# Optimization experiments

Hardware: AMD Instinct MI355X
Metric: run time of the kernel (lower is better)

The kernel has to match this reference:

```python
import jax, jax.numpy as jnp
import numpy as np

N_EMBD = 1024
N_HEAD = 16
HEAD_SIZE = 64


def setup_inputs() -> dict:
    key = jax.random.key(0)
    ks = jax.random.split(key, 6)
    B, T, C, H, D = 2, 2048, N_EMBD, N_HEAD, HEAD_SIZE
    s = 1.0 / np.sqrt(C)
    x = jax.random.normal(ks[0], (B, T, C), dtype=jnp.float32)
    Wq = jax.random.normal(ks[1], (H, C, D), dtype=jnp.float32) * s
    Wk = jax.random.normal(ks[2], (H, C, D), dtype=jnp.float32) * s
    Wv = jax.random.normal(ks[3], (H, C, D), dtype=jnp.float32) * s
    Wo = jax.random.normal(ks[4], (H * D, C), dtype=jnp.float32) * (1.0 / np.sqrt(H * D))
    bo = jax.random.normal(ks[5], (C,), dtype=jnp.float32) * 0.01
    return {"x": x, "Wq": Wq, "Wk": Wk, "Wv": Wv, "Wo": Wo, "bo": bo}


def reference(x, Wq, Wk, Wv, Wo, bo):
    B, T, C = x.shape
    H, _, D = Wq.shape
    # Per-head projections, batched across heads: [B,H,T,D]
    q = jnp.einsum('btc,hcd->bhtd', x, Wq)
    k = jnp.einsum('btc,hcd->bhtd', x, Wk)
    v = jnp.einsum('btc,hcd->bhtd', x, Wv)
    # NOTE: original scales by sqrt(C) = sqrt(n_embd), not sqrt(head_size)
    scale = 1.0 / jnp.sqrt(jnp.float32(C))
    att = jnp.einsum('bhtd,bhsd->bhts', q, k) * scale  # [B,H,T,T]
    causal = jnp.tril(jnp.ones((T, T), dtype=bool))
    att = jnp.where(causal, att, -jnp.inf)
    att = jax.nn.softmax(att, axis=-1)
    # dropout omitted (eval mode / deterministic reference)
    out = jnp.einsum('bhts,bhsd->bhtd', att, v)  # [B,H,T,D]
    out = out.transpose(0, 2, 1, 3).reshape(B, T, H * D)
    return out @ Wo + bo
```

## Files before the change

kernel.cpp:

```cpp
#include <hip/hip_runtime.h>
#include <hip/hip_bf16.h>


typedef __hip_bfloat16 bf16;
typedef __bf16 v8bf __attribute__((ext_vector_type(8)));
typedef float  v4f  __attribute__((ext_vector_type(4)));
typedef unsigned long long u64;
typedef unsigned int u32;

#define MFMA16(a, b, c) __builtin_amdgcn_mfma_f32_16x16x32_bf16((a), (b), (c), 0, 0, 0)

__device__ __forceinline__ bf16 f2b(float x) { return __float2bfloat16(x); }
__device__ __forceinline__ __bf16 f2braw(float x) {
  bf16 t = __float2bfloat16(x);
  return *reinterpret_cast<__bf16*>(&t);
}
__device__ __forceinline__ unsigned short f2bu(float x) {
  bf16 t = __float2bfloat16(x);
  return *reinterpret_cast<unsigned short*>(&t);
}

__device__ __forceinline__ void load16_lds(const bf16* gptr, const bf16* lptr) {
  __builtin_amdgcn_global_load_lds(
      (const __attribute__((address_space(1))) u32*)gptr,
      (__attribute__((address_space(3))) u32*)lptr, 16, 0, 0);
}

__global__ __launch_bounds__(256) void prep_kernel(
    const float* __restrict__ x,
    const float* __restrict__ Wq, const float* __restrict__ Wk,
    const float* __restrict__ Wv, const float* __restrict__ Wo,
    bf16* __restrict__ xb, bf16* __restrict__ wt, bf16* __restrict__ wot)
{
  __shared__ float Lt[32][33];
  const int bid = blockIdx.x, tid = threadIdx.x;

  if (bid < 2048) {
    size_t i = ((size_t)bid * 256 + tid) * 8;
    float4 f0 = *(const float4*)(x + i);
    float4 f1 = *(const float4*)(x + i + 4);
    v8bf v;
    v[0] = f2braw(f0.x); v[1] = f2braw(f0.y); v[2] = f2braw(f0.z); v[3] = f2braw(f0.w);
    v[4] = f2braw(f1.x); v[5] = f2braw(f1.y); v[6] = f2braw(f1.z); v[7] = f2braw(f1.w);
    *(v8bf*)(xb + i) = v;
    return;
  }
  const int tx = tid & 31, ty = tid >> 5;
  if (bid < 5120) {
    const int idx = bid - 2048;
    const int z = idx >> 6, rem = idx & 63;
    const int p = z >> 4, h = z & 15;
    const float* ib = ((p == 0) ? Wq : (p == 1) ? Wk : Wv) + (size_t)h * 65536;
    bf16* ob = wt + (size_t)z * 65536;
    const int j0 = (rem & 1) * 32, i0 = (rem >> 1) * 32;
    #pragma unroll
    for (int r = 0; r < 4; ++r)
      Lt[ty + 8 * r][tx] = ib[(size_t)(i0 + ty + 8 * r) * 64 + j0 + tx];
    __syncthreads();
    #pragma unroll
    for (int r = 0; r < 4; ++r)
      ob[(size_t)(j0 + ty + 8 * r) * 1024 + i0 + tx] = f2b(Lt[tx][ty + 8 * r]);
  } else {
    const int idx = bid - 5120;
    const int j0 = (idx & 31) * 32, i0 = (idx >> 5) * 32;
    #pragma unroll
    for (int r = 0; r < 4; ++r)
      Lt[ty + 8 * r][tx] = Wo[(size_t)(i0 + ty + 8 * r) * 1024 + j0 + tx];
    __syncthreads();
    #pragma unroll
    for (int r = 0; r < 4; ++r)
      wot[(size_t)(j0 + ty + 8 * r) * 1024 + i0 + tx] = f2b(Lt[tx][ty + 8 * r]);
  }
}

__global__ __launch_bounds__(256) void qkv_gemm_kernel(
    const bf16* __restrict__ xb, const bf16* __restrict__ wt,
    bf16* __restrict__ qkv)
{
  __shared__ __align__(16) bf16 Ash[2][128][32];
  __shared__ __align__(16) bf16 Bsh[2][128][32];

  const int mt = blockIdx.x, nt = blockIdx.y;
  const int tid = threadIdx.x, w = tid >> 6, lane = tid & 63;
  const int ln = lane & 15, quad = lane >> 4;
  const int wm = w >> 1, wn = w & 1;
  const int m0 = mt * 128, n0 = nt * 128;

  const v4f vzero = {0.f, 0.f, 0.f, 0.f};
  v4f acc[4][4];
  #pragma unroll
  for (int mf = 0; mf < 4; ++mf)
    #pragma unroll
    for (int nf = 0; nf < 4; ++nf) acc[mf][nf] = vzero;

  const int srow = lane >> 2, sseg = (lane & 3) * 8;
  const bf16* ga = xb + (size_t)(m0 + 32 * w + srow) * 1024 + sseg;
  const bf16* gb = wt + (size_t)(n0 + 32 * w + srow) * 1024 + sseg;

  {
    load16_lds(ga,             &Ash[0][32 * w][0]);
    load16_lds(ga + 16 * 1024, &Ash[0][32 * w + 16][0]);
    load16_lds(gb,             &Bsh[0][32 * w][0]);
    load16_lds(gb + 16 * 1024, &Bsh[0][32 * w + 16][0]);
  }

  for (int kt = 0; kt < 32; ++kt) {
    const int buf = kt & 1;
    __syncthreads();

    v8bf af[4], bfv[4];
    #pragma unroll
    for (int mf = 0; mf < 4; ++mf)
      af[mf] = *(const v8bf*)&Ash[buf][wm * 64 + mf * 16 + ln][quad * 8];
    #pragma unroll
    for (int nf = 0; nf < 4; ++nf)
      bfv[nf] = *(const v8bf*)&Bsh[buf][wn * 64 + nf * 16 + ln][quad * 8];

    if (kt < 31) {
      const int k0 = (kt + 1) * 32, nb = buf ^ 1;
      load16_lds(ga + k0,             &Ash[nb][32 * w][0]);
      load16_lds(ga + 16 * 1024 + k0, &Ash[nb][32 * w + 16][0]);
      load16_lds(gb + k0,             &Bsh[nb][32 * w][0]);
      load16_lds(gb + 16 * 1024 + k0, &Bsh[nb][32 * w + 16][0]);
    }

    #pragma unroll
    for (int mf = 0; mf < 4; ++mf)
      #pragma unroll
      for (int nf = 0; nf < 4; ++nf)
        acc[mf][nf] = MFMA16(af[mf], bfv[nf], acc[mf][nf]);
  }

  const int jcol0 = n0 + wn * 64;
  const int p = jcol0 >> 10;
  const int h = (jcol0 >> 6) & 15;
  const float scale = (p == 0) ? 0.03125f : 1.0f;

  if (p < 2) {
    bf16* base = qkv + (size_t)p * 4194304 + (size_t)h * 262144;
    #pragma unroll
    for (int mf = 0; mf < 4; ++mf)
      #pragma unroll
      for (int nf = 0; nf < 4; ++nf) {
        int d = nf * 16 + ln;
        #pragma unroll
        for (int r = 0; r < 4; ++r) {
          int m = m0 + wm * 64 + mf * 16 + quad * 4 + r;
          base[(size_t)m * 64 + d] = f2b(acc[mf][nf][r] * scale);
        }
      }
  } else {
    bf16* vb = qkv + (size_t)2 * 4194304 + (size_t)h * 262144;
    #pragma unroll
    for (int mf = 0; mf < 4; ++mf) {
      int mrow = m0 + wm * 64 + mf * 16 + quad * 4;
      int bi = mrow >> 11, t0 = mrow & 2047;
      #pragma unroll
      for (int nf = 0; nf < 4; ++nf) {
        int d = nf * 16 + ln;
        u64 pk = (u64)f2bu(acc[mf][nf][0]) |
                 ((u64)f2bu(acc[mf][nf][1]) << 16) |
                 ((u64)f2bu(acc[mf][nf][2]) << 32) |
                 ((u64)f2bu(acc[mf][nf][3]) << 48);
        *(u64*)(vb + (size_t)bi * 131072 + (size_t)d * 2048 + t0) = pk;
      }
    }
  }
}

__global__ __launch_bounds__(256, 2) void attn_kernel(
    const bf16* __restrict__ qkv, bf16* __restrict__ att)
{
  __shared__ __align__(16) bf16 Ksh[2][64][64];
  __shared__ __align__(16) bf16 Vsh[2][64][64];

  const int fid = blockIdx.x;
  const int pairid = fid >> 5;
  const int grp = fid & 31;
  const int b = grp >> 4, h = grp & 15;

  const int tid = threadIdx.x, w = tid >> 6, lane = tid & 63;
  const int ln = lane & 15, quad = lane >> 4;

  const bf16* qbase  = qkv + (size_t)h * 262144 + (size_t)b * 131072;
  const bf16* kbase  = qbase + 4194304;
  const bf16* vtbase = qbase + 8388608;

  const int l8 = lane & 7, r8 = lane >> 3;
  const int slot = l8 ^ r8;
  const int p0 = w * 16 + r8, p1 = p0 + 8;
  const int kp0 = (p0 & 32) | ((p0 & 12) << 1) | ((p0 & 16) >> 2) | (p0 & 3);
  const int kp1 = (p1 & 32) | ((p1 & 12) << 1) | ((p1 & 16) >> 2) | (p1 & 3);
  const bf16* gk0 = kbase + kp0 * 64 + slot * 8;
  const bf16* gk1 = kbase + kp1 * 64 + slot * 8;
  const bf16* gv0 = vtbase + (w * 16 + r8) * 2048 + slot * 8;
  const bf16* gv1 = gv0 + 8 * 2048;

  const int sw = ln & 7;
  const int c0 = ((quad    ) ^ sw) * 8;
  const int c1 = ((quad + 4) ^ sw) * 8;
  const int rowoff = ln * 64;

  v8bf vone;
  {
    unsigned short u = 0x3F80;
    __bf16 e = *reinterpret_cast<__bf16*>(&u);
    #pragma unroll
    for (int j = 0; j < 8; ++j) vone[j] = e;
  }
  const v4f vzero = {0.f, 0.f, 0.f, 0.f};
  const float NEG = -30000.0f;

  #define STAGE(KB, BUF) {                                       \
    load16_lds(gk0 + (KB) * 4096, &Ksh[BUF][w * 16][0]);         \
    load16_lds(gk1 + (KB) * 4096, &Ksh[BUF][w * 16 + 8][0]);     \
    load16_lds(gv0 + (KB) * 64,   &Vsh[BUF][w * 16][0]);         \
    load16_lds(gv1 + (KB) * 64,   &Vsh[BUF][w * 16 + 8][0]); }

  #pragma unroll 1
  for (int half = 0; half < 2; ++half) {
    const int mt = half ? (31 - pairid) : pairid;
    const int row0 = mt * 64;
    const int wrow = row0 + w * 16;
    const int qg = wrow + ln;

    v8bf aq[2];
    #pragma unroll
    for (int ks = 0; ks < 2; ++ks)
      aq[ks] = *(const v8bf*)(qbase + (size_t)(wrow + ln) * 64 + ks * 32 + quad * 8);

    v4f o[4], lacc;
    lacc = vzero;
    #pragma unroll
    for (int dt = 0; dt < 4; ++dt) o[dt] = vzero;

    if (half) __syncthreads();
    STAGE(0, 0)

    const int kb_end = mt;
    for (int kb = 0; kb <= kb_end; ++kb) {
      const int buf = kb & 1;
      __syncthreads();

      v8bf kf[2][4], vf[2][4];
      const bf16* kr = &Ksh[buf][0][0];
      const bf16* vr = &Vsh[buf][0][0];
      #pragma unroll
      for (int nf = 0; nf < 4; ++nf) {
        kf[0][nf] = *(const v8bf*)(kr + nf * 1024 + rowoff + c0);
        kf[1][nf] = *(const v8bf*)(kr + nf * 1024 + rowoff + c1);
        vf[0][nf] = *(const v8bf*)(vr + nf * 1024 + rowoff + c0);
        vf[1][nf] = *(const v8bf*)(vr + nf * 1024 + rowoff + c1);
      }

      if (kb < kb_end) STAGE(kb + 1, buf ^ 1)

      v4f s[4];
      #pragma unroll
      for (int nf = 0; nf < 4; ++nf) s[nf] = vzero;
      #pragma unroll
      for (int ks = 0; ks < 2; ++ks)
        #pragma unroll
        for (int nf = 0; nf < 4; ++nf)
          s[nf] = MFMA16(kf[ks][nf], aq[ks], s[nf]);

      if (kb == kb_end) {
        #pragma unroll
        for (int nf = 0; nf < 4; ++nf) {
          const int kc = kb * 64 + (nf >> 1) * 32 + quad * 8 + (nf & 1) * 4;
          #pragma unroll
          for (int r = 0; r < 4; ++r)
            if (kc + r > qg) s[nf][r] = NEG;
        }
      }

      v8bf pa[2];
      #pragma unroll
      for (int ks = 0; ks < 2; ++ks)
        #pragma unroll
        for (int hh = 0; hh < 2; ++hh)
          #pragma unroll
          for (int r = 0; r < 4; ++r)
            pa[ks][hh * 4 + r] = f2braw(__expf(s[2 * ks + hh][r]));

      lacc = MFMA16(pa[0], vone, lacc);
      lacc = MFMA16(pa[1], vone, lacc);
      #pragma unroll
      for (int ks = 0; ks < 2; ++ks)
        #pragma unroll
        for (int dt = 0; dt < 4; ++dt)
          o[dt] = MFMA16(pa[ks], vf[ks][dt], o[dt]);
    }

    v4f inv;
    #pragma unroll
    for (int r = 0; r < 4; ++r) inv[r] = 1.0f / lacc[r];
    #pragma unroll
    for (int dt = 0; dt < 4; ++dt)
      #pragma unroll
      for (int r = 0; r < 4; ++r) {
        int m = b * 2048 + wrow + quad * 4 + r;
        att[(size_t)m * 1024 + h * 64 + dt * 16 + ln] = f2b(o[dt][r] * inv[r]);
      }
  }
  #undef STAGE
}

__global__ __launch_bounds__(256) void out_gemm_kernel(
    const bf16* __restrict__ att, const bf16* __restrict__ wot,
    const float* __restrict__ bo, float* __restrict__ out)
{
  __shared__ __align__(16) bf16 Ash[2][128][32];
  __shared__ __align__(16) bf16 Bsh[2][64][32];

  const int mt = blockIdx.x, nt = blockIdx.y;
  const int tid = threadIdx.x, w = tid >> 6, lane = tid & 63;
  const int ln = lane & 15, quad = lane >> 4;
  const int wm = w >> 1, wn = w & 1;
  const int m0 = mt * 128, n0 = nt * 64;

  const v4f vzero = {0.f, 0.f, 0.f, 0.f};
  v4f acc[4][2];
  #pragma unroll
  for (int mf = 0; mf < 4; ++mf)
    #pragma unroll
    for (int nf = 0; nf < 2; ++nf) acc[mf][nf] = vzero;

  const int srow = lane >> 2, sseg = (lane & 3) * 8;
  const bf16* ga = att + (size_t)(m0 + 32 * w + srow) * 1024 + sseg;
  const bf16* gb = wot + (size_t)(n0 + 16 * w + srow) * 1024 + sseg;

  {
    load16_lds(ga,             &Ash[0][32 * w][0]);
    load16_lds(ga + 16 * 1024, &Ash[0][32 * w + 16][0]);
    load16_lds(gb,             &Bsh[0][16 * w][0]);
  }

  for (int kt = 0; kt < 32; ++kt) {
    const int buf = kt & 1;
    __syncthreads();

    v8bf af[4], bfv[2];
    #pragma unroll
    for (int mf = 0; mf < 4; ++mf)
      af[mf] = *(const v8bf*)&Ash[buf][wm * 64 + mf * 16 + ln][quad * 8];
    #pragma unroll
    for (int nf = 0; nf < 2; ++nf)
      bfv[nf] = *(const v8bf*)&Bsh[buf][wn * 32 + nf * 16 + ln][quad * 8];

    if (kt < 31) {
      const int k0 = (kt + 1) * 32, nb = buf ^ 1;
      load16_lds(ga + k0,             &Ash[nb][32 * w][0]);
      load16_lds(ga + 16 * 1024 + k0, &Ash[nb][32 * w + 16][0]);
      load16_lds(gb + k0,             &Bsh[nb][16 * w][0]);
    }

    #pragma unroll
    for (int mf = 0; mf < 4; ++mf)
      #pragma unroll
      for (int nf = 0; nf < 2; ++nf)
        acc[mf][nf] = MFMA16(af[mf], bfv[nf], acc[mf][nf]);
  }

  #pragma unroll
  for (int nf = 0; nf < 2; ++nf) {
    int j = n0 + wn * 32 + nf * 16 + ln;
    float bias = bo[j];
    #pragma unroll
    for (int mf = 0; mf < 4; ++mf)
      #pragma unroll
      for (int r = 0; r < 4; ++r) {
        int m = m0 + wm * 64 + mf * 16 + quad * 4 + r;
        out[(size_t)m * 1024 + j] = acc[mf][nf][r] + bias;
      }
  }
}

extern "C" void kernel_launch(void* const* d_in, const int* in_sizes, int n_in,
                              void* d_out, int out_size, void* d_ws, size_t ws_size,
                              hipStream_t stream) {
  const float* x  = (const float*)d_in[0];
  const float* Wq = (const float*)d_in[1];
  const float* Wk = (const float*)d_in[2];
  const float* Wv = (const float*)d_in[3];
  const float* Wo = (const float*)d_in[4];
  const float* bo = (const float*)d_in[5];
  float* out = (float*)d_out;

  bf16* xb  = (bf16*)d_ws;
  bf16* wt  = xb + 4194304;
  bf16* wot = xb + 7340032;
  bf16* qkv = xb + 8388608;
  bf16* att = xb + 20971520;

  prep_kernel<<<6144, 256, 0, stream>>>(x, Wq, Wk, Wv, Wo, xb, wt, wot);
  qkv_gemm_kernel<<<dim3(32, 24), 256, 0, stream>>>(xb, wt, qkv);
  attn_kernel<<<512, 256, 0, stream>>>(qkv, att);
  out_gemm_kernel<<<dim3(32, 16), 256, 0, stream>>>(att, wot, bo, out);
}
```

Measured before the change: 165.7 us.

## Give each attention wave two query row-chunks and fold log2e into Q scale

The attention kernel now runs two waves per block instead of four, and each wave handles 32 query rows as two 16-row chunks. The K/V fragments read from LDS are reused across both chunks, which halves LDS traffic per MFMA. Staging loads per thread double to cover the tile with fewer threads. The Q scale now includes log2(e), so the softmax uses exp2f instead of __expf. Registers per wave rise and there are fewer waves per block to hide latency.

```diff
diff --git a/kernel.cpp b/kernel.cpp
--- a/kernel.cpp
+++ b/kernel.cpp
@@ -134,7 +134,7 @@
   const int jcol0 = n0 + wn * 64;
   const int p = jcol0 >> 10;
   const int h = (jcol0 >> 6) & 15;
-  const float scale = (p == 0) ? 0.03125f : 1.0f;
+  const float scale = (p == 0) ? 0.0450841149f : 1.0f;
 
   if (p < 2) {
     bf16* base = qkv + (size_t)p * 4194304 + (size_t)h * 262144;
@@ -168,7 +168,7 @@
   }
 }
 
-__global__ __launch_bounds__(256, 2) void attn_kernel(
+__global__ __launch_bounds__(128, 2) void attn_kernel(
     const bf16* __restrict__ qkv, bf16* __restrict__ att)
 {
   __shared__ __align__(16) bf16 Ksh[2][64][64];
@@ -188,13 +188,15 @@
 
   const int l8 = lane & 7, r8 = lane >> 3;
   const int slot = l8 ^ r8;
-  const int p0 = w * 16 + r8, p1 = p0 + 8;
-  const int kp0 = (p0 & 32) | ((p0 & 12) << 1) | ((p0 & 16) >> 2) | (p0 & 3);
-  const int kp1 = (p1 & 32) | ((p1 & 12) << 1) | ((p1 & 16) >> 2) | (p1 & 3);
-  const bf16* gk0 = kbase + kp0 * 64 + slot * 8;
-  const bf16* gk1 = kbase + kp1 * 64 + slot * 8;
-  const bf16* gv0 = vtbase + (w * 16 + r8) * 2048 + slot * 8;
-  const bf16* gv1 = gv0 + 8 * 2048;
+  const bf16* gk[4];
+  const bf16* gv[4];
+  #pragma unroll
+  for (int i = 0; i < 4; ++i) {
+    const int p = w * 32 + 8 * i + r8;
+    const int kp = (p & 32) | ((p & 12) << 1) | ((p & 16) >> 2) | (p & 3);
+    gk[i] = kbase + kp * 64 + slot * 8;
+    gv[i] = vtbase + p * 2048 + slot * 8;
+  }
 
   const int sw = ln & 7;
   const int c0 = ((quad    ) ^ sw) * 8;
@@ -212,27 +214,36 @@
   const float NEG = -30000.0f;
 
   #define STAGE(KB, BUF) {                                       \
-    load16_lds(gk0 + (KB) * 4096, &Ksh[BUF][w * 16][0]);         \
-    load16_lds(gk1 + (KB) * 4096, &Ksh[BUF][w * 16 + 8][0]);     \
-    load16_lds(gv0 + (KB) * 64,   &Vsh[BUF][w * 16][0]);         \
-    load16_lds(gv1 + (KB) * 64,   &Vsh[BUF][w * 16 + 8][0]); }
+    load16_lds(gk[0] + (KB) * 4096, &Ksh[BUF][w * 32][0]);       \
+    load16_lds(gk[1] + (KB) * 4096, &Ksh[BUF][w * 32 + 8][0]);   \
+    load16_lds(gk[2] + (KB) * 4096, &Ksh[BUF][w * 32 + 16][0]);  \
+    load16_lds(gk[3] + (KB) * 4096, &Ksh[BUF][w * 32 + 24][0]);  \
+    load16_lds(gv[0] + (KB) * 64,   &Vsh[BUF][w * 32][0]);       \
+    load16_lds(gv[1] + (KB) * 64,   &Vsh[BUF][w * 32 + 8][0]);   \
+    load16_lds(gv[2] + (KB) * 64,   &Vsh[BUF][w * 32 + 16][0]);  \
+    load16_lds(gv[3] + (KB) * 64,   &Vsh[BUF][w * 32 + 24][0]); }
 
   #pragma unroll 1
   for (int half = 0; half < 2; ++half) {
     const int mt = half ? (31 - pairid) : pairid;
     const int row0 = mt * 64;
-    const int wrow = row0 + w * 16;
-    const int qg = wrow + ln;
-
-    v8bf aq[2];
-    #pragma unroll
-    for (int ks = 0; ks < 2; ++ks)
-      aq[ks] = *(const v8bf*)(qbase + (size_t)(wrow + ln) * 64 + ks * 32 + quad * 8);
-
-    v4f o[4], lacc;
-    lacc = vzero;
-    #pragma unroll
-    for (int dt = 0; dt < 4; ++dt) o[dt] = vzero;
+    const int wrow = row0 + w * 32;
+
+    v8bf aq[2][2];
+    #pragma unroll
+    for (int mc = 0; mc < 2; ++mc)
+      #pragma unroll
+      for (int ks = 0; ks < 2; ++ks)
+        aq[mc][ks] = *(const v8bf*)(qbase +
+            (size_t)(wrow + mc * 16 + ln) * 64 + ks * 32 + quad * 8);
+
+    v4f o[2][4], lacc[2];
+    #pragma unroll
+    for (int mc = 0; mc < 2; ++mc) {
+      lacc[mc] = vzero;
+      #pragma unroll
+      for (int dt = 0; dt < 4; ++dt) o[mc][dt] = vzero;
+    }
 
     if (half) __syncthreads();
     STAGE(0, 0)
@@ -255,53 +266,61 @@
 
       if (kb < kb_end) STAGE(kb + 1, buf ^ 1)
 
-      v4f s[4];
-      #pragma unroll
-      for (int nf = 0; nf < 4; ++nf) s[nf] = vzero;
-      #pragma unroll
-      for (int ks = 0; ks < 2; ++ks)
-        #pragma unroll
-        for (int nf = 0; nf < 4; ++nf)
-          s[nf] = MFMA16(kf[ks][nf], aq[ks], s[nf]);
-
-      if (kb == kb_end) {
-        #pragma unroll
-        for (int nf = 0; nf < 4; ++nf) {
-          const int kc = kb * 64 + (nf >> 1) * 32 + quad * 8 + (nf & 1) * 4;
+      #pragma unroll
+      for (int mc = 0; mc < 2; ++mc) {
+        v4f s[4];
+        #pragma unroll
+        for (int nf = 0; nf < 4; ++nf) s[nf] = vzero;
+        #pragma unroll
+        for (int ks = 0; ks < 2; ++ks)
           #pragma unroll
-          for (int r = 0; r < 4; ++r)
-            if (kc + r > qg) s[nf][r] = NEG;
+          for (int nf = 0; nf < 4; ++nf)
+            s[nf] = MFMA16(kf[ks][nf], aq[mc][ks], s[nf]);
+
+        const int qg = wrow + mc * 16 + ln;
+        if (kb == kb_end) {
+          #pragma unroll
+          for (int nf = 0; nf < 4; ++nf) {
+            const int kc = kb * 64 + (nf >> 1) * 32 + quad * 8 + (nf & 1) * 4;
+            #pragma unroll
+            for (int r = 0; r < 4; ++r)
+              if (kc + r > qg) s[nf][r] = NEG;
+          }
         }
+
+        v8bf pa[2];
+        #pragma unroll
+        for (int ks = 0; ks < 2; ++ks)
+          #pragma unroll
+          for (int hh = 0; hh < 2; ++hh)
+            #pragma unroll
+            for (int r = 0; r < 4; ++r)
+              pa[ks][hh * 4 + r] = f2braw(exp2f(s[2 * ks + hh][r]));
+
+        lacc[mc] = MFMA16(pa[0], vone, lacc[mc]);
+        lacc[mc] = MFMA16(pa[1], vone, lacc[mc]);
+        #pragma unroll
+        for (int ks = 0; ks < 2; ++ks)
+          #pragma unroll
+          for (int dt = 0; dt < 4; ++dt)
+            o[mc][dt] = MFMA16(pa[ks], vf[ks][dt], o[mc][dt]);
       }
-
-      v8bf pa[2];
-      #pragma unroll
-      for (int ks = 0; ks < 2; ++ks)
-        #pragma unroll
-        for (int hh = 0; hh < 2; ++hh)
-          #pragma unroll
-          for (int r = 0; r < 4; ++r)
-            pa[ks][hh * 4 + r] = f2braw(__expf(s[2 * ks + hh][r]));
-
-      lacc = MFMA16(pa[0], vone, lacc);
-      lacc = MFMA16(pa[1], vone, lacc);
-      #pragma unroll
-      for (int ks = 0; ks < 2; ++ks)
-        #pragma unroll
-        for (int dt = 0; dt < 4; ++dt)
-          o[dt] = MFMA16(pa[ks], vf[ks][dt], o[dt]);
-    }
-
-    v4f inv;
-    #pragma unroll
-    for (int r = 0; r < 4; ++r) inv[r] = 1.0f / lacc[r];
-    #pragma unroll
-    for (int dt = 0; dt < 4; ++dt)
-      #pragma unroll
-      for (int r = 0; r < 4; ++r) {
-        int m = b * 2048 + wrow + quad * 4 + r;
-        att[(size_t)m * 1024 + h * 64 + dt * 16 + ln] = f2b(o[dt][r] * inv[r]);
-      }
+    }
+
+    #pragma unroll
+    for (int mc = 0; mc < 2; ++mc) {
+      v4f inv;
+      #pragma unroll
+      for (int r = 0; r < 4; ++r) inv[r] = 1.0f / lacc[mc][r];
+      #pragma unroll
+      for (int dt = 0; dt < 4; ++dt)
+        #pragma unroll
+        for (int r = 0; r < 4; ++r) {
+          int m = b * 2048 + wrow + mc * 16 + quad * 4 + r;
+          att[(size_t)m * 1024 + h * 64 + dt * 16 + ln] =
+              f2b(o[mc][dt][r] * inv[r]);
+        }
+    }
   }
   #undef STAGE
 }
@@ -395,6 +414,6 @@
 
   prep_kernel<<<6144, 256, 0, stream>>>(x, Wq, Wk, Wv, Wo, xb, wt, wot);
   qkv_gemm_kernel<<<dim3(32, 24), 256, 0, stream>>>(xb, wt, qkv);
-  attn_kernel<<<512, 256, 0, stream>>>(qkv, att);
+  attn_kernel<<<512, 128, 0, stream>>>(qkv, att);
   out_gemm_kernel<<<dim3(32, 16), 256, 0, stream>>>(att, wot, bo, out);
 }
```

Measured after the change: 187.5 us. +13.1%, slower.

## Split attention query-tile pairs into separate blocks and use exp2 with folded log2e scale

Applied to the files above, without the earlier changes.

Each attention block now handles one 64-row query tile instead of a paired light and heavy tile, and the grid doubles to 1024 blocks. Tiles are ordered heavy-first in interleaved groups to balance the causal workload, and occupancy is raised to 4 blocks per CU. The Q scale now folds in log2(e) so softmax can use exp2f, packing to bf16 goes through v_cvt_pk_bf16_f32, and MFMA phases are wrapped in s_setprio. The trade-off is more block launches and repeated prologues in exchange for better load balance and latency hiding.

```diff
diff --git a/kernel.cpp b/kernel.cpp
--- a/kernel.cpp
+++ b/kernel.cpp
@@ -134,7 +134,7 @@
   const int jcol0 = n0 + wn * 64;
   const int p = jcol0 >> 10;
   const int h = (jcol0 >> 6) & 15;
-  const float scale = (p == 0) ? 0.03125f : 1.0f;
+  const float scale = (p == 0) ? 0.0450841149f : 1.0f;
 
   if (p < 2) {
     bf16* base = qkv + (size_t)p * 4194304 + (size_t)h * 262144;
@@ -168,14 +168,17 @@
   }
 }
 
-__global__ __launch_bounds__(256, 2) void attn_kernel(
+__global__ __launch_bounds__(256, 4) void attn_kernel(
     const bf16* __restrict__ qkv, bf16* __restrict__ att)
 {
   __shared__ __align__(16) bf16 Ksh[2][64][64];
   __shared__ __align__(16) bf16 Vsh[2][64][64];
 
   const int fid = blockIdx.x;
-  const int pairid = fid >> 5;
+  const int j = fid >> 5;
+  const int jr = j & 7, jq = j >> 3;
+  const int mt = (jq == 0) ? (31 - jr) : (jq == 1) ? (8 + jr)
+               : (jq == 2) ? (23 - jr) : jr;
   const int grp = fid & 31;
   const int b = grp >> 4, h = grp & 15;
 
@@ -193,7 +196,7 @@
   const int kp1 = (p1 & 32) | ((p1 & 12) << 1) | ((p1 & 16) >> 2) | (p1 & 3);
   const bf16* gk0 = kbase + kp0 * 64 + slot * 8;
   const bf16* gk1 = kbase + kp1 * 64 + slot * 8;
-  const bf16* gv0 = vtbase + (w * 16 + r8) * 2048 + slot * 8;
+  const bf16* gv0 = vtbase + p0 * 2048 + slot * 8;
   const bf16* gv1 = gv0 + 8 * 2048;
 
   const int sw = ln & 7;
@@ -206,7 +209,7 @@
     unsigned short u = 0x3F80;
     __bf16 e = *reinterpret_cast<__bf16*>(&u);
     #pragma unroll
-    for (int j = 0; j < 8; ++j) vone[j] = e;
+    for (int jj = 0; jj < 8; ++jj) vone[jj] = e;
   }
   const v4f vzero = {0.f, 0.f, 0.f, 0.f};
   const float NEG = -30000.0f;
@@ -217,93 +220,100 @@
     load16_lds(gv0 + (KB) * 64,   &Vsh[BUF][w * 16][0]);         \
     load16_lds(gv1 + (KB) * 64,   &Vsh[BUF][w * 16 + 8][0]); }
 
-  #pragma unroll 1
-  for (int half = 0; half < 2; ++half) {
-    const int mt = half ? (31 - pairid) : pairid;
-    const int row0 = mt * 64;
-    const int wrow = row0 + w * 16;
-    const int qg = wrow + ln;
-
-    v8bf aq[2];
+  const int wrow = mt * 64 + w * 16;
+  const int qg = wrow + ln;
+
+  v8bf aq[2];
+  #pragma unroll
+  for (int ks = 0; ks < 2; ++ks)
+    aq[ks] = *(const v8bf*)(qbase + (size_t)(wrow + ln) * 64 + ks * 32 + quad * 8);
+
+  v4f o[4], lacc;
+  lacc = vzero;
+  #pragma unroll
+  for (int dt = 0; dt < 4; ++dt) o[dt] = vzero;
+
+  STAGE(0, 0)
+
+  const int kb_end = mt;
+  for (int kb = 0; kb <= kb_end; ++kb) {
+    const int buf = kb & 1;
+    __syncthreads();
+
+    v8bf kf[2][4], vf[2][4];
+    const bf16* kr = &Ksh[buf][0][0];
+    const bf16* vr = &Vsh[buf][0][0];
+    #pragma unroll
+    for (int nf = 0; nf < 4; ++nf) {
+      kf[0][nf] = *(const v8bf*)(kr + nf * 1024 + rowoff + c0);
+      kf[1][nf] = *(const v8bf*)(kr + nf * 1024 + rowoff + c1);
+      vf[0][nf] = *(const v8bf*)(vr + nf * 1024 + rowoff + c0);
+      vf[1][nf] = *(const v8bf*)(vr + nf * 1024 + rowoff + c1);
+    }
+
+    if (kb < kb_end) STAGE(kb + 1, buf ^ 1)
+
+    __builtin_amdgcn_s_setprio(1);
+    v4f s[4];
+    #pragma unroll
+    for (int nf = 0; nf < 4; ++nf) s[nf] = vzero;
     #pragma unroll
     for (int ks = 0; ks < 2; ++ks)
-      aq[ks] = *(const v8bf*)(qbase + (size_t)(wrow + ln) * 64 + ks * 32 + quad * 8);
-
-    v4f o[4], lacc;
-    lacc = vzero;
-    #pragma unroll
-    for (int dt = 0; dt < 4; ++dt) o[dt] = vzero;
-
-    if (half) __syncthreads();
-    STAGE(0, 0)
-
-    const int kb_end = mt;
-    for (int kb = 0; kb <= kb_end; ++kb) {
-      const int buf = kb & 1;
-      __syncthreads();
-
-      v8bf kf[2][4], vf[2][4];
-      const bf16* kr = &Ksh[buf][0][0];
-      const bf16* vr = &Vsh[buf][0][0];
+      #pragma unroll
+      for (int nf = 0; nf < 4; ++nf)
+        s[nf] = MFMA16(kf[ks][nf], aq[ks], s[nf]);
+    __builtin_amdgcn_s_setprio(0);
+
+    if (kb == kb_end) {
       #pragma unroll
       for (int nf = 0; nf < 4; ++nf) {
-        kf[0][nf] = *(const v8bf*)(kr + nf * 1024 + rowoff + c0);
-        kf[1][nf] = *(const v8bf*)(kr + nf * 1024 + rowoff + c1);
-        vf[0][nf] = *(const v8bf*)(vr + nf * 1024 + rowoff + c0);
-        vf[1][nf] = *(const v8bf*)(vr + nf * 1024 + rowoff + c1);
+        const int kc = kb * 64 + (nf >> 1) * 32 + quad * 8 + (nf & 1) * 4;
+        #pragma unroll
+        for (int r = 0; r < 4; ++r)
+          if (kc + r > qg) s[nf][r] = NEG;
       }
-
-      if (kb < kb_end) STAGE(kb + 1, buf ^ 1)
-
-      v4f s[4];
-      #pragma unroll
-      for (int nf = 0; nf < 4; ++nf) s[nf] = vzero;
-      #pragma unroll
-      for (int ks = 0; ks < 2; ++ks)
+    }
+
+    float ex[4][4];
+    #pragma unroll
+    for (int nf = 0; nf < 4; ++nf)
+      #pragma unroll
+      for (int r = 0; r < 4; ++r)
+        ex[nf][r] = exp2f(s[nf][r]);
+
+    union { u32 w[4]; v8bf v; } pu[2];
+    #pragma unroll
+    for (int ks = 0; ks < 2; ++ks)
+      #pragma unroll
+      for (int hh = 0; hh < 2; ++hh)
         #pragma unroll
-        for (int nf = 0; nf < 4; ++nf)
-          s[nf] = MFMA16(kf[ks][nf], aq[ks], s[nf]);
-
-      if (kb == kb_end) {
-        #pragma unroll
-        for (int nf = 0; nf < 4; ++nf) {
-          const int kc = kb * 64 + (nf >> 1) * 32 + quad * 8 + (nf & 1) * 4;
-          #pragma unroll
-          for (int r = 0; r < 4; ++r)
-            if (kc + r > qg) s[nf][r] = NEG;
-        }
-      }
-
-      v8bf pa[2];
-      #pragma unroll
-      for (int ks = 0; ks < 2; ++ks)
-        #pragma unroll
-        for (int hh = 0; hh < 2; ++hh)
-          #pragma unroll
-          for (int r = 0; r < 4; ++r)
-            pa[ks][hh * 4 + r] = f2braw(__expf(s[2 * ks + hh][r]));
-
-      lacc = MFMA16(pa[0], vone, lacc);
-      lacc = MFMA16(pa[1], vone, lacc);
-      #pragma unroll
-      for (int ks = 0; ks < 2; ++ks)
-        #pragma unroll
-        for (int dt = 0; dt < 4; ++dt)
-          o[dt] = MFMA16(pa[ks], vf[ks][dt], o[dt]);
-    }
-
-    v4f inv;
-    #pragma unroll
-    for (int r = 0; r < 4; ++r) inv[r] = 1.0f / lacc[r];
-    #pragma unroll
-    for (int dt = 0; dt < 4; ++dt)
-      #pragma unroll
-      for (int r = 0; r < 4; ++r) {
-        int m = b * 2048 + wrow + quad * 4 + r;
-        att[(size_t)m * 1024 + h * 64 + dt * 16 + ln] = f2b(o[dt][r] * inv[r]);
-      }
+        for (int wi = 0; wi < 2; ++wi)
+          asm("v_cvt_pk_bf16_f32 %0, %1, %2"
+              : "=v"(pu[ks].w[hh * 2 + wi])
+              : "v"(ex[2 * ks + hh][2 * wi]), "v"(ex[2 * ks + hh][2 * wi + 1]));
+
+    __builtin_amdgcn_s_setprio(1);
+    lacc = MFMA16(pu[0].v, vone, lacc);
+    lacc = MFMA16(pu[1].v, vone, lacc);
+    #pragma unroll
+    for (int ks = 0; ks < 2; ++ks)
+      #pragma unroll
+      for (int dt = 0; dt < 4; ++dt)
+        o[dt] = MFMA16(pu[ks].v, vf[ks][dt], o[dt]);
+    __builtin_amdgcn_s_setprio(0);
   }
   #undef STAGE
+
+  v4f inv;
+  #pragma unroll
+  for (int r = 0; r < 4; ++r) inv[r] = 1.0f / lacc[r];
+  #pragma unroll
+  for (int dt = 0; dt < 4; ++dt)
+    #pragma unroll
+    for (int r = 0; r < 4; ++r) {
+      int m = b * 2048 + wrow + quad * 4 + r;
+      att[(size_t)m * 1024 + h * 64 + dt * 16 + ln] = f2b(o[dt][r] * inv[r]);
+    }
 }
 
 __global__ __launch_bounds__(256) void out_gemm_kernel(
@@ -395,6 +405,6 @@
 
   prep_kernel<<<6144, 256, 0, stream>>>(x, Wq, Wk, Wv, Wo, xb, wt, wot);
   qkv_gemm_kernel<<<dim3(32, 24), 256, 0, stream>>>(xb, wt, qkv);
-  attn_kernel<<<512, 256, 0, stream>>>(qkv, att);
+  attn_kernel<<<1024, 256, 0, stream>>>(qkv, att);
   out_gemm_kernel<<<dim3(32, 16), 256, 0, stream>>>(att, wot, bo, out);
 }
```

After: 168.7 us. About the same (+1.8%).
